# Kernel tuning notes

Hardware: AMD Instinct MI355X
Metric: run time of the kernel (lower is better)

Reference implementation:

```python
import jax, jax.numpy as jnp
import numpy as np

D_MODEL = 2048
N_HEADS = 16
D_HEAD = D_MODEL // N_HEADS
FF = 4 * D_MODEL
ROPE_BASE = 10000.0


def setup_inputs() -> dict:
    key = jax.random.key(0)
    ks = jax.random.split(key, 12)
    s = 0.02
    B, S = 2, 2048
    return {
        "x": jax.random.normal(ks[0], (B, S, D_MODEL), dtype=jnp.float32),
        # torch Linear layout: [out_features, in_features]
        "w_qkv": jax.random.normal(ks[1], (3 * D_MODEL, D_MODEL), dtype=jnp.float32) * s,
        "w_proj": jax.random.normal(ks[2], (D_MODEL, D_MODEL), dtype=jnp.float32) * s,
        "b_proj": jnp.zeros((D_MODEL,), dtype=jnp.float32),
        "w_ff1": jax.random.normal(ks[3], (FF, D_MODEL), dtype=jnp.float32) * s,
        "b_ff1": jnp.zeros((FF,), dtype=jnp.float32),
        "w_ff2": jax.random.normal(ks[4], (D_MODEL, FF), dtype=jnp.float32) * s,
        "b_ff2": jnp.zeros((D_MODEL,), dtype=jnp.float32),
        "g1": jnp.ones((D_MODEL,), dtype=jnp.float32),
        "beta1": jnp.zeros((D_MODEL,), dtype=jnp.float32),
        "g2": jnp.ones((D_MODEL,), dtype=jnp.float32),
        "beta2": jnp.zeros((D_MODEL,), dtype=jnp.float32),
    }


def _layer_norm(x, g, b, eps=1e-5):
    mu = jnp.mean(x, axis=-1, keepdims=True)
    var = jnp.var(x, axis=-1, keepdims=True)
    return (x - mu) * jax.lax.rsqrt(var + eps) * g + b


def _rope_cos_sin(seq_len, dtype):
    inv_freq = 1.0 / (ROPE_BASE ** (jnp.arange(0, D_HEAD, 2, dtype=jnp.float32) / D_HEAD))
    t = jnp.arange(seq_len, dtype=jnp.float32)
    freqs = jnp.einsum("i,j->ij", t, inv_freq)  # [S, D_HEAD//2]
    emb = jnp.concatenate([freqs, freqs], axis=-1)  # [S, D_HEAD]
    return jnp.cos(emb).astype(dtype), jnp.sin(emb).astype(dtype)


def _rotate_half(x):
    x1, x2 = x[..., : D_HEAD // 2], x[..., D_HEAD // 2 :]
    return jnp.concatenate([-x2, x1], axis=-1)


def reference(x, w_qkv, w_proj, b_proj, w_ff1, b_ff1, w_ff2, b_ff2, g1, beta1, g2, beta2):
    B, S, _ = x.shape
    # --- attention block ---
    h = _layer_norm(x, g1, beta1)
    qkv = h @ w_qkv.T  # [B,S,3D]
    xq, xk, xv = jnp.split(qkv, 3, axis=-1)
    xq = xq.reshape(B, S, N_HEADS, D_HEAD)
    xk = xk.reshape(B, S, N_HEADS, D_HEAD)
    xv = xv.reshape(B, S, N_HEADS, D_HEAD)
    cos, sin = _rope_cos_sin(S, x.dtype)
    cos = cos[None, :, None, :]  # [1,S,1,Dh]
    sin = sin[None, :, None, :]
    xq = xq * cos + _rotate_half(xq) * sin
    xk = xk * cos + _rotate_half(xk) * sin
    # SDPA, causal
    scale = 1.0 / jnp.sqrt(jnp.asarray(D_HEAD, dtype=x.dtype))
    scores = jnp.einsum("bqhd,bkhd->bhqk", xq, xk) * scale  # [B,H,S,S]
    causal = jnp.tril(jnp.ones((S, S), dtype=bool))
    scores = jnp.where(causal[None, None], scores, jnp.finfo(x.dtype).min)
    att = jax.nn.softmax(scores, axis=-1)
    out = jnp.einsum("bhqk,bkhd->bqhd", att, xv).reshape(B, S, D_MODEL)
    att_out = out @ w_proj.T + b_proj
    x = x + att_out
    # --- feed-forward block (exact GELU, matching nn.GELU default) ---
    h = _layer_norm(x, g2, beta2)
    ff = jax.nn.gelu(h @ w_ff1.T + b_ff1, approximate=False) @ w_ff2.T + b_ff2
    return x + ff
```

## Files before the change

kernel.cpp:

```cpp
#include <hip/hip_runtime.h>
#include <hip/hip_bf16.h>
#include <cmath>

#define D_MODEL 2048
#define N_HEADS 16
#define D_HEAD  128
#define FFDIM   8192
#define BATCH   2
#define SEQ     2048
#define TOKENS  (BATCH * SEQ)

using bf16 = __hip_bfloat16;
typedef __bf16 v8bf __attribute__((ext_vector_type(8)));
typedef float  v4f  __attribute__((ext_vector_type(4)));

__device__ inline __bf16 f2b(float f) {
    bf16 h = __float2bfloat16(f);
    return *reinterpret_cast<__bf16*>(&h);
}

__global__ __launch_bounds__(256) void cast_kernel(const float* __restrict__ in,
                                                   bf16* __restrict__ out, int n4) {
    int i = blockIdx.x * 256 + threadIdx.x;
    if (i < n4) {
        float4 f = ((const float4*)in)[i];
        int o = i * 4;
        out[o + 0] = __float2bfloat16(f.x);
        out[o + 1] = __float2bfloat16(f.y);
        out[o + 2] = __float2bfloat16(f.z);
        out[o + 3] = __float2bfloat16(f.w);
    }
}

__global__ __launch_bounds__(256) void ln_kernel(const float* __restrict__ x,
                                                 const float* __restrict__ g,
                                                 const float* __restrict__ b,
                                                 bf16* __restrict__ out) {
    int row = blockIdx.x;
    int t = threadIdx.x;
    const float* xr = x + (size_t)row * D_MODEL;
    float v[8];
    float s = 0.f, s2 = 0.f;
#pragma unroll
    for (int i = 0; i < 8; i++) {
        float val = xr[t + 256 * i];
        v[i] = val;
        s += val;
        s2 += val * val;
    }
#pragma unroll
    for (int off = 32; off > 0; off >>= 1) {
        s  += __shfl_down(s, off, 64);
        s2 += __shfl_down(s2, off, 64);
    }
    __shared__ float ws1[4], ws2[4];
    int wv = t >> 6;
    if ((t & 63) == 0) { ws1[wv] = s; ws2[wv] = s2; }
    __syncthreads();
    float fs  = ws1[0] + ws1[1] + ws1[2] + ws1[3];
    float fs2 = ws2[0] + ws2[1] + ws2[2] + ws2[3];
    float mean = fs * (1.0f / D_MODEL);
    float var  = fs2 * (1.0f / D_MODEL) - mean * mean;
    float rstd = rsqrtf(var + 1e-5f);
    bf16* orow = out + (size_t)row * D_MODEL;
#pragma unroll
    for (int i = 0; i < 8; i++) {
        int c = t + 256 * i;
        orow[c] = __float2bfloat16((v[i] - mean) * rstd * g[c] + b[c]);
    }
}

__global__ __launch_bounds__(256) void rope_kernel(float* __restrict__ qkv) {
    int unit = blockIdx.x * 4 + (threadIdx.x >> 6);
    int j = threadIdx.x & 63;
    int h = unit & (N_HEADS - 1);
    int tok = unit >> 4;
    int pos = tok & (SEQ - 1);
    float invf = powf(10000.0f, -(float)j / 64.0f);
    float ang = (float)pos * invf;
    float c = cosf(ang), s = sinf(ang);
    size_t base = (size_t)tok * (3 * D_MODEL) + h * D_HEAD;
    float q1 = qkv[base + j], q2 = qkv[base + j + 64];
    qkv[base + j]      = q1 * c - q2 * s;
    qkv[base + j + 64] = q2 * c + q1 * s;
    size_t kb = base + D_MODEL;
    float k1 = qkv[kb + j], k2 = qkv[kb + j + 64];
    qkv[kb + j]      = k1 * c - k2 * s;
    qkv[kb + j + 64] = k2 * c + k1 * s;
}

__global__ __launch_bounds__(256) void vt_kernel(const float* __restrict__ qkv,
                                                 bf16* __restrict__ vt) {
    __shared__ float tile[32][65];
    int bh = blockIdx.x;
    int k0 = blockIdx.y * 64;
    int d0 = blockIdx.z * 32;
    int b = bh >> 4, h = bh & 15;
    int t = threadIdx.x;
    const float* src = qkv + ((size_t)b * SEQ + k0) * (3 * D_MODEL) + 2 * D_MODEL + h * D_HEAD + d0;
#pragma unroll
    for (int i = 0; i < 8; i++) {
        int e = t + 256 * i;
        int kr = e >> 5, dc = e & 31;
        tile[dc][kr] = src[(size_t)kr * (3 * D_MODEL) + dc];
    }
    __syncthreads();
    bf16* dst = vt + ((size_t)bh * D_HEAD + d0) * SEQ + k0;
#pragma unroll
    for (int i = 0; i < 8; i++) {
        int e = t + 256 * i;
        int dr = e >> 6, kc = e & 63;
        dst[(size_t)dr * SEQ + kc] = __float2bfloat16(tile[dr][kc]);
    }
}

#define KS_STRIDE 136
#define VT_STRIDE 72
#define PS_STRIDE 72

__global__ __launch_bounds__(256) void flash_attn(const float* __restrict__ qkv,
                                                  const bf16* __restrict__ vt,
                                                  bf16* __restrict__ att) {
    __shared__ __align__(16) bf16 Ks[64 * KS_STRIDE];
    __shared__ __align__(16) bf16 Vts[D_HEAD * VT_STRIDE];
    __shared__ __align__(16) bf16 Ps[4 * 16 * PS_STRIDE];

    int bh = blockIdx.x;
    int qt = (int)gridDim.y - 1 - (int)blockIdx.y;
    int b = bh >> 4, h = bh & 15;
    int t = threadIdx.x, wave = t >> 6, lane = t & 63;
    int lr = lane & 15, lq = lane >> 4;

    const float* qp = qkv + ((size_t)b * SEQ + qt * 64 + wave * 16 + lr) * (3 * D_MODEL) + h * D_HEAD;
    v8bf aq[4];
#pragma unroll
    for (int c = 0; c < 4; c++) {
        const float4* q4 = (const float4*)(qp + c * 32 + lq * 8);
        float4 qa = q4[0], qb = q4[1];
        aq[c][0] = f2b(qa.x * 0.08838834764831845f);
        aq[c][1] = f2b(qa.y * 0.08838834764831845f);
        aq[c][2] = f2b(qa.z * 0.08838834764831845f);
        aq[c][3] = f2b(qa.w * 0.08838834764831845f);
        aq[c][4] = f2b(qb.x * 0.08838834764831845f);
        aq[c][5] = f2b(qb.y * 0.08838834764831845f);
        aq[c][6] = f2b(qb.z * 0.08838834764831845f);
        aq[c][7] = f2b(qb.w * 0.08838834764831845f);
    }

    float m_r[4], l_r[4];
    v4f O[8] = {};
#pragma unroll
    for (int r = 0; r < 4; r++) { m_r[r] = -1e30f; l_r[r] = 0.f; }

    int n_tiles = qt + 1;
    for (int kt = 0; kt < n_tiles; kt++) {
        int kv0 = kt * 64;
        __syncthreads();
        {
            const float* kbase = qkv + ((size_t)b * SEQ + kv0) * (3 * D_MODEL) + D_MODEL + h * D_HEAD;
#pragma unroll
            for (int i = 0; i < 8; i++) {
                int e4 = t + 256 * i;
                int kr = e4 >> 5, c4 = (e4 & 31) * 4;
                float4 f = *(const float4*)(kbase + (size_t)kr * (3 * D_MODEL) + c4);
                bf16* dst = &Ks[kr * KS_STRIDE + c4];
                dst[0] = __float2bfloat16(f.x);
                dst[1] = __float2bfloat16(f.y);
                dst[2] = __float2bfloat16(f.z);
                dst[3] = __float2bfloat16(f.w);
            }
            const bf16* vbase = vt + (size_t)bh * D_HEAD * SEQ + kv0;
#pragma unroll
            for (int i = 0; i < 4; i++) {
                int e8 = t + 256 * i;
                int dr = e8 >> 3, k8 = (e8 & 7) * 8;
                *(uint4*)&Vts[dr * VT_STRIDE + k8] = *(const uint4*)(vbase + (size_t)dr * SEQ + k8);
            }
        }
        __syncthreads();

        v4f sc[4];
#pragma unroll
        for (int nt = 0; nt < 4; nt++) {
            v4f a = {};
#pragma unroll
            for (int c = 0; c < 4; c++) {
                v8bf bk = *(const v8bf*)&Ks[(nt * 16 + lr) * KS_STRIDE + c * 32 + lq * 8];
                a = __builtin_amdgcn_mfma_f32_16x16x32_bf16(aq[c], bk, a, 0, 0, 0);
            }
            sc[nt] = a;
        }
        if (kt == n_tiles - 1) {
#pragma unroll
            for (int nt = 0; nt < 4; nt++)
#pragma unroll
                for (int r = 0; r < 4; r++) {
                    int cl = nt * 16 + lr, rl = wave * 16 + lq * 4 + r;
                    if (cl > rl) sc[nt][r] = -1e30f;
                }
        }
        float mt[4];
#pragma unroll
        for (int r = 0; r < 4; r++) {
            float v = fmaxf(fmaxf(sc[0][r], sc[1][r]), fmaxf(sc[2][r], sc[3][r]));
#pragma unroll
            for (int mk = 8; mk >= 1; mk >>= 1) v = fmaxf(v, __shfl_xor(v, mk, 64));
            mt[r] = v;
        }
        float alpha[4];
#pragma unroll
        for (int r = 0; r < 4; r++) {
            float mn = fmaxf(m_r[r], mt[r]);
            alpha[r] = __expf(m_r[r] - mn);
            m_r[r] = mn;
        }
        bf16* pw = &Ps[wave * 16 * PS_STRIDE];
        float rs[4] = {0.f, 0.f, 0.f, 0.f};
#pragma unroll
        for (int nt = 0; nt < 4; nt++)
#pragma unroll
            for (int r = 0; r < 4; r++) {
                float p = __expf(sc[nt][r] - m_r[r]);
                rs[r] += p;
                pw[(lq * 4 + r) * PS_STRIDE + nt * 16 + lr] = __float2bfloat16(p);
            }
#pragma unroll
        for (int r = 0; r < 4; r++) {
            float v = rs[r];
#pragma unroll
            for (int mk = 8; mk >= 1; mk >>= 1) v += __shfl_xor(v, mk, 64);
            l_r[r] = l_r[r] * alpha[r] + v;
        }
#pragma unroll
        for (int jt = 0; jt < 8; jt++)
#pragma unroll
            for (int r = 0; r < 4; r++) O[jt][r] *= alpha[r];

        asm volatile("s_waitcnt lgkmcnt(0)" ::: "memory");

        v8bf ap[2];
#pragma unroll
        for (int c = 0; c < 2; c++)
            ap[c] = *(const v8bf*)&pw[lr * PS_STRIDE + c * 32 + lq * 8];
#pragma unroll
        for (int jt = 0; jt < 8; jt++) {
#pragma unroll
            for (int c = 0; c < 2; c++) {
                v8bf bv = *(const v8bf*)&Vts[(jt * 16 + lr) * VT_STRIDE + c * 32 + lq * 8];
                O[jt] = __builtin_amdgcn_mfma_f32_16x16x32_bf16(ap[c], bv, O[jt], 0, 0, 0);
            }
        }
    }

    float inv[4];
#pragma unroll
    for (int r = 0; r < 4; r++) inv[r] = 1.0f / l_r[r];
#pragma unroll
    for (int jt = 0; jt < 8; jt++)
#pragma unroll
        for (int r = 0; r < 4; r++) {
            size_t idx = ((size_t)b * SEQ + qt * 64 + wave * 16 + lq * 4 + r) * D_MODEL + h * D_HEAD + jt * 16 + lr;
            att[idx] = __float2bfloat16(O[jt][r] * inv[r]);
        }
}

#define BM 128
#define BN 128
#define BK 32

template <int EPI>
__global__ __launch_bounds__(256) void gemm_bt(const bf16* __restrict__ A,
                                               const bf16* __restrict__ W,
                                               const float* __restrict__ bias,
                                               const float* __restrict__ res,
                                               float* __restrict__ outF,
                                               bf16* __restrict__ outB,
                                               int M, int N, int K) {
    __shared__ __align__(16) bf16 As[BM * BK];
    __shared__ __align__(16) bf16 Bs[BN * BK];
    int t = threadIdx.x;
    int wave = t >> 6, lane = t & 63;
    int wm = (wave >> 1) * 64;
    int wn = (wave & 1) * 64;
    int lr = lane & 15;
    int lq = lane >> 4;
    int row0 = blockIdx.y * BM;
    int col0 = blockIdx.x * BN;
    int lr4 = lane >> 2;
    int lc8 = (lane & 3) * 8;

    v4f acc[4][4] = {};

    for (int k0 = 0; k0 < K; k0 += BK) {
#pragma unroll
        for (int u = 0; u < 2; u++) {
            int c = wave * 2 + u;
            const bf16* ga = A + (size_t)(row0 + c * 16 + lr4) * K + k0 + lc8;
            __builtin_amdgcn_global_load_lds(
                (const __attribute__((address_space(1))) void*)ga,
                (__attribute__((address_space(3))) void*)&As[c * 512], 16, 0, 0);
            const bf16* gb = W + (size_t)(col0 + c * 16 + lr4) * K + k0 + lc8;
            __builtin_amdgcn_global_load_lds(
                (const __attribute__((address_space(1))) void*)gb,
                (__attribute__((address_space(3))) void*)&Bs[c * 512], 16, 0, 0);
        }
        __syncthreads();
        v8bf af[4], bfr[4];
#pragma unroll
        for (int i = 0; i < 4; i++) {
            af[i]  = *(const v8bf*)(&As[(wm + i * 16 + lr) * BK + lq * 8]);
            bfr[i] = *(const v8bf*)(&Bs[(wn + i * 16 + lr) * BK + lq * 8]);
        }
#pragma unroll
        for (int i = 0; i < 4; i++)
#pragma unroll
            for (int j = 0; j < 4; j++)
                acc[i][j] = __builtin_amdgcn_mfma_f32_16x16x32_bf16(af[i], bfr[j], acc[i][j], 0, 0, 0);
        __syncthreads();
    }

#pragma unroll
    for (int i = 0; i < 4; i++) {
#pragma unroll
        for (int j = 0; j < 4; j++) {
#pragma unroll
            for (int r = 0; r < 4; r++) {
                int grow = row0 + wm + i * 16 + lq * 4 + r;
                int gcol = col0 + wn + j * 16 + lr;
                float c = acc[i][j][r];
                size_t idx = (size_t)grow * N + gcol;
                if (EPI == 0) {
                    outF[idx] = c;
                } else if (EPI == 1) {
                    outF[idx] = c + bias[gcol] + res[idx];
                } else {
                    c += bias[gcol];
                    float gel = 0.5f * c * (1.0f + erff(c * 0.7071067811865475f));
                    outB[idx] = __float2bfloat16(gel);
                }
            }
        }
    }
}

extern "C" void kernel_launch(void* const* d_in, const int* in_sizes, int n_in,
                              void* d_out, int out_size, void* d_ws, size_t ws_size,
                              hipStream_t stream) {
    const float* x      = (const float*)d_in[0];
    const float* w_qkv  = (const float*)d_in[1];
    const float* w_proj = (const float*)d_in[2];
    const float* b_proj = (const float*)d_in[3];
    const float* w_ff1  = (const float*)d_in[4];
    const float* b_ff1  = (const float*)d_in[5];
    const float* w_ff2  = (const float*)d_in[6];
    const float* b_ff2  = (const float*)d_in[7];
    const float* g1     = (const float*)d_in[8];
    const float* be1    = (const float*)d_in[9];
    const float* g2     = (const float*)d_in[10];
    const float* be2    = (const float*)d_in[11];
    float* out = (float*)d_out;

    char* ws = (char*)d_ws;
    size_t off = 0;
    auto alloc = [&](size_t bytes) {
        void* p = ws + off;
        off += (bytes + 255) & ~(size_t)255;
        return p;
    };
    bf16*  wqkv_b  = (bf16*)alloc((size_t)3 * D_MODEL * D_MODEL * sizeof(bf16));
    bf16*  wproj_b = (bf16*)alloc((size_t)D_MODEL * D_MODEL * sizeof(bf16));
    bf16*  wff1_b  = (bf16*)alloc((size_t)FFDIM * D_MODEL * sizeof(bf16));
    bf16*  wff2_b  = (bf16*)alloc((size_t)D_MODEL * FFDIM * sizeof(bf16));
    float* qkv_f   = (float*)alloc((size_t)TOKENS * 3 * D_MODEL * sizeof(float));
    bf16*  act_b   = (bf16*)alloc((size_t)TOKENS * D_MODEL * sizeof(bf16));
    float* x2_f    = (float*)alloc((size_t)TOKENS * D_MODEL * sizeof(float));
    bf16*  ff1_b   = (bf16*)qkv_f;
    bf16*  vt_g    = (bf16*)x2_f;

    cast_kernel<<<(3 * D_MODEL * D_MODEL / 4 + 255) / 256, 256, 0, stream>>>(w_qkv, wqkv_b, 3 * D_MODEL * D_MODEL / 4);
    cast_kernel<<<(D_MODEL * D_MODEL / 4 + 255) / 256, 256, 0, stream>>>(w_proj, wproj_b, D_MODEL * D_MODEL / 4);
    cast_kernel<<<(FFDIM * D_MODEL / 4 + 255) / 256, 256, 0, stream>>>(w_ff1, wff1_b, FFDIM * D_MODEL / 4);
    cast_kernel<<<(D_MODEL * FFDIM / 4 + 255) / 256, 256, 0, stream>>>(w_ff2, wff2_b, D_MODEL * FFDIM / 4);

    ln_kernel<<<TOKENS, 256, 0, stream>>>(x, g1, be1, act_b);

    gemm_bt<0><<<dim3(3 * D_MODEL / BN, TOKENS / BM), 256, 0, stream>>>(
        act_b, wqkv_b, nullptr, nullptr, qkv_f, nullptr, TOKENS, 3 * D_MODEL, D_MODEL);

    rope_kernel<<<TOKENS * N_HEADS / 4, 256, 0, stream>>>(qkv_f);

    vt_kernel<<<dim3(BATCH * N_HEADS, SEQ / 64, D_HEAD / 32), 256, 0, stream>>>(qkv_f, vt_g);

    flash_attn<<<dim3(BATCH * N_HEADS, SEQ / 64), 256, 0, stream>>>(qkv_f, vt_g, act_b);

    gemm_bt<1><<<dim3(D_MODEL / BN, TOKENS / BM), 256, 0, stream>>>(
        act_b, wproj_b, b_proj, x, x2_f, nullptr, TOKENS, D_MODEL, D_MODEL);

    ln_kernel<<<TOKENS, 256, 0, stream>>>(x2_f, g2, be2, act_b);

    gemm_bt<2><<<dim3(FFDIM / BN, TOKENS / BM), 256, 0, stream>>>(
        act_b, wff1_b, b_ff1, nullptr, nullptr, ff1_b, TOKENS, FFDIM, D_MODEL);

    gemm_bt<1><<<dim3(D_MODEL / BN, TOKENS / BM), 256, 0, stream>>>(
        ff1_b, wff2_b, b_ff2, x2_f, out, nullptr, TOKENS, D_MODEL, FFDIM);

    (void)in_sizes; (void)n_in; (void)out_size; (void)ws_size;
}
```

Before: 1.108 ms.

## Store QKV in bf16, fold softmax scale into RoPE, and swizzle GEMM block order

The QKV GEMM now writes bf16 instead of fp32 through a new epilogue. RoPE, the V transpose and flash attention read bf16 directly, and the softmax scale is folded into the RoPE pass, so attention loads Q and K with plain 16-byte vector copies instead of converting on the fly. This halves QKV memory traffic and drops the conversion work inside attention. Separately, all GEMMs remap block IDs with an XCD-aware, grouped panel swizzle to improve L2 reuse across the MI355X chiplets. Rounding Q and K to bf16 before RoPE adds a little extra precision loss.

```diff
diff --git a/kernel.cpp b/kernel.cpp
--- a/kernel.cpp
+++ b/kernel.cpp
@@ -13,11 +13,6 @@
 using bf16 = __hip_bfloat16;
 typedef __bf16 v8bf __attribute__((ext_vector_type(8)));
 typedef float  v4f  __attribute__((ext_vector_type(4)));
-
-__device__ inline __bf16 f2b(float f) {
-    bf16 h = __float2bfloat16(f);
-    return *reinterpret_cast<__bf16*>(&h);
-}
 
 __global__ __launch_bounds__(256) void cast_kernel(const float* __restrict__ in,
                                                    bf16* __restrict__ out, int n4) {
@@ -70,7 +65,7 @@
     }
 }
 
-__global__ __launch_bounds__(256) void rope_kernel(float* __restrict__ qkv) {
+__global__ __launch_bounds__(256) void rope_kernel(bf16* __restrict__ qkv) {
     int unit = blockIdx.x * 4 + (threadIdx.x >> 6);
     int j = threadIdx.x & 63;
     int h = unit & (N_HEADS - 1);
@@ -79,17 +74,18 @@
     float invf = powf(10000.0f, -(float)j / 64.0f);
     float ang = (float)pos * invf;
     float c = cosf(ang), s = sinf(ang);
+    const float sc = 0.08838834764831845f;
     size_t base = (size_t)tok * (3 * D_MODEL) + h * D_HEAD;
-    float q1 = qkv[base + j], q2 = qkv[base + j + 64];
-    qkv[base + j]      = q1 * c - q2 * s;
-    qkv[base + j + 64] = q2 * c + q1 * s;
+    float q1 = __bfloat162float(qkv[base + j]), q2 = __bfloat162float(qkv[base + j + 64]);
+    qkv[base + j]      = __float2bfloat16((q1 * c - q2 * s) * sc);
+    qkv[base + j + 64] = __float2bfloat16((q2 * c + q1 * s) * sc);
     size_t kb = base + D_MODEL;
-    float k1 = qkv[kb + j], k2 = qkv[kb + j + 64];
-    qkv[kb + j]      = k1 * c - k2 * s;
-    qkv[kb + j + 64] = k2 * c + k1 * s;
-}
-
-__global__ __launch_bounds__(256) void vt_kernel(const float* __restrict__ qkv,
+    float k1 = __bfloat162float(qkv[kb + j]), k2 = __bfloat162float(qkv[kb + j + 64]);
+    qkv[kb + j]      = __float2bfloat16(k1 * c - k2 * s);
+    qkv[kb + j + 64] = __float2bfloat16(k2 * c + k1 * s);
+}
+
+__global__ __launch_bounds__(256) void vt_kernel(const bf16* __restrict__ qkv,
                                                  bf16* __restrict__ vt) {
     __shared__ float tile[32][65];
     int bh = blockIdx.x;
@@ -97,12 +93,12 @@
     int d0 = blockIdx.z * 32;
     int b = bh >> 4, h = bh & 15;
     int t = threadIdx.x;
-    const float* src = qkv + ((size_t)b * SEQ + k0) * (3 * D_MODEL) + 2 * D_MODEL + h * D_HEAD + d0;
+    const bf16* src = qkv + ((size_t)b * SEQ + k0) * (3 * D_MODEL) + 2 * D_MODEL + h * D_HEAD + d0;
 #pragma unroll
     for (int i = 0; i < 8; i++) {
         int e = t + 256 * i;
         int kr = e >> 5, dc = e & 31;
-        tile[dc][kr] = src[(size_t)kr * (3 * D_MODEL) + dc];
+        tile[dc][kr] = __bfloat162float(src[(size_t)kr * (3 * D_MODEL) + dc]);
     }
     __syncthreads();
     bf16* dst = vt + ((size_t)bh * D_HEAD + d0) * SEQ + k0;
@@ -118,7 +114,7 @@
 #define VT_STRIDE 72
 #define PS_STRIDE 72
 
-__global__ __launch_bounds__(256) void flash_attn(const float* __restrict__ qkv,
+__global__ __launch_bounds__(256) void flash_attn(const bf16* __restrict__ qkv,
                                                   const bf16* __restrict__ vt,
                                                   bf16* __restrict__ att) {
     __shared__ __align__(16) bf16 Ks[64 * KS_STRIDE];
@@ -131,21 +127,11 @@
     int t = threadIdx.x, wave = t >> 6, lane = t & 63;
     int lr = lane & 15, lq = lane >> 4;
 
-    const float* qp = qkv + ((size_t)b * SEQ + qt * 64 + wave * 16 + lr) * (3 * D_MODEL) + h * D_HEAD;
+    const bf16* qp = qkv + ((size_t)b * SEQ + qt * 64 + wave * 16 + lr) * (3 * D_MODEL) + h * D_HEAD;
     v8bf aq[4];
 #pragma unroll
-    for (int c = 0; c < 4; c++) {
-        const float4* q4 = (const float4*)(qp + c * 32 + lq * 8);
-        float4 qa = q4[0], qb = q4[1];
-        aq[c][0] = f2b(qa.x * 0.08838834764831845f);
-        aq[c][1] = f2b(qa.y * 0.08838834764831845f);
-        aq[c][2] = f2b(qa.z * 0.08838834764831845f);
-        aq[c][3] = f2b(qa.w * 0.08838834764831845f);
-        aq[c][4] = f2b(qb.x * 0.08838834764831845f);
-        aq[c][5] = f2b(qb.y * 0.08838834764831845f);
-        aq[c][6] = f2b(qb.z * 0.08838834764831845f);
-        aq[c][7] = f2b(qb.w * 0.08838834764831845f);
-    }
+    for (int c = 0; c < 4; c++)
+        aq[c] = *(const v8bf*)(qp + c * 32 + lq * 8);
 
     float m_r[4], l_r[4];
     v4f O[8] = {};
@@ -157,17 +143,12 @@
         int kv0 = kt * 64;
         __syncthreads();
         {
-            const float* kbase = qkv + ((size_t)b * SEQ + kv0) * (3 * D_MODEL) + D_MODEL + h * D_HEAD;
-#pragma unroll
-            for (int i = 0; i < 8; i++) {
-                int e4 = t + 256 * i;
-                int kr = e4 >> 5, c4 = (e4 & 31) * 4;
-                float4 f = *(const float4*)(kbase + (size_t)kr * (3 * D_MODEL) + c4);
-                bf16* dst = &Ks[kr * KS_STRIDE + c4];
-                dst[0] = __float2bfloat16(f.x);
-                dst[1] = __float2bfloat16(f.y);
-                dst[2] = __float2bfloat16(f.z);
-                dst[3] = __float2bfloat16(f.w);
+            const bf16* kbase = qkv + ((size_t)b * SEQ + kv0) * (3 * D_MODEL) + D_MODEL + h * D_HEAD;
+#pragma unroll
+            for (int i = 0; i < 4; i++) {
+                int e = t + 256 * i;
+                int kr = e >> 4, c8 = (e & 15) * 8;
+                *(uint4*)&Ks[kr * KS_STRIDE + c8] = *(const uint4*)(kbase + (size_t)kr * (3 * D_MODEL) + c8);
             }
             const bf16* vbase = vt + (size_t)bh * D_HEAD * SEQ + kv0;
 #pragma unroll
@@ -284,8 +265,20 @@
     int wn = (wave & 1) * 64;
     int lr = lane & 15;
     int lq = lane >> 4;
-    int row0 = blockIdx.y * BM;
-    int col0 = blockIdx.x * BN;
+
+    int nbx = gridDim.x;
+    int bid = (int)blockIdx.y * nbx + (int)blockIdx.x;
+    int per = (nbx * (int)gridDim.y) >> 3;
+    int lbid = (bid & 7) * per + (bid >> 3);
+    const int GM = 8;
+    int pw = GM * nbx;
+    int panel = lbid / pw;
+    int rem = lbid - panel * pw;
+    int bm = panel * GM + (rem & (GM - 1));
+    int bn = rem >> 3;
+    int row0 = bm * BM;
+    int col0 = bn * BN;
+
     int lr4 = lane >> 2;
     int lc8 = (lane & 3) * 8;
 
@@ -333,10 +326,12 @@
                     outF[idx] = c;
                 } else if (EPI == 1) {
                     outF[idx] = c + bias[gcol] + res[idx];
-                } else {
+                } else if (EPI == 2) {
                     c += bias[gcol];
                     float gel = 0.5f * c * (1.0f + erff(c * 0.7071067811865475f));
                     outB[idx] = __float2bfloat16(gel);
+                } else {
+                    outB[idx] = __float2bfloat16(c);
                 }
             }
         }
@@ -371,10 +366,10 @@
     bf16*  wproj_b = (bf16*)alloc((size_t)D_MODEL * D_MODEL * sizeof(bf16));
     bf16*  wff1_b  = (bf16*)alloc((size_t)FFDIM * D_MODEL * sizeof(bf16));
     bf16*  wff2_b  = (bf16*)alloc((size_t)D_MODEL * FFDIM * sizeof(bf16));
-    float* qkv_f   = (float*)alloc((size_t)TOKENS * 3 * D_MODEL * sizeof(float));
+    bf16*  qkv_b   = (bf16*)alloc((size_t)TOKENS * FFDIM * sizeof(bf16));
+    bf16*  ff1_b   = qkv_b;
     bf16*  act_b   = (bf16*)alloc((size_t)TOKENS * D_MODEL * sizeof(bf16));
     float* x2_f    = (float*)alloc((size_t)TOKENS * D_MODEL * sizeof(float));
-    bf16*  ff1_b   = (bf16*)qkv_f;
     bf16*  vt_g    = (bf16*)x2_f;
 
     cast_kernel<<<(3 * D_MODEL * D_MODEL / 4 + 255) / 256, 256, 0, stream>>>(w_qkv, wqkv_b, 3 * D_MODEL * D_MODEL / 4);
@@ -384,14 +379,14 @@
 
     ln_kernel<<<TOKENS, 256, 0, stream>>>(x, g1, be1, act_b);
 
-    gemm_bt<0><<<dim3(3 * D_MODEL / BN, TOKENS / BM), 256, 0, stream>>>(
-        act_b, wqkv_b, nullptr, nullptr, qkv_f, nullptr, TOKENS, 3 * D_MODEL, D_MODEL);
-
-    rope_kernel<<<TOKENS * N_HEADS / 4, 256, 0, stream>>>(qkv_f);
-
-    vt_kernel<<<dim3(BATCH * N_HEADS, SEQ / 64, D_HEAD / 32), 256, 0, stream>>>(qkv_f, vt_g);
-
-    flash_attn<<<dim3(BATCH * N_HEADS, SEQ / 64), 256, 0, stream>>>(qkv_f, vt_g, act_b);
+    gemm_bt<3><<<dim3(3 * D_MODEL / BN, TOKENS / BM), 256, 0, stream>>>(
+        act_b, wqkv_b, nullptr, nullptr, nullptr, qkv_b, TOKENS, 3 * D_MODEL, D_MODEL);
+
+    rope_kernel<<<TOKENS * N_HEADS / 4, 256, 0, stream>>>(qkv_b);
+
+    vt_kernel<<<dim3(BATCH * N_HEADS, SEQ / 64, D_HEAD / 32), 256, 0, stream>>>(qkv_b, vt_g);
+
+    flash_attn<<<dim3(BATCH * N_HEADS, SEQ / 64), 256, 0, stream>>>(qkv_b, vt_g, act_b);
 
     gemm_bt<1><<<dim3(D_MODEL / BN, TOKENS / BM), 256, 0, stream>>>(
         act_b, wproj_b, b_proj, x, x2_f, nullptr, TOKENS, D_MODEL, D_MODEL);
```

Result: faster. 1.042 ms (-5.9%).
